# Performance work log

Measured on AMD Instinct MI355X. Metric: run time of the kernel, lower is better.

## Reference

```python
import jax, jax.numpy as jnp
import numpy as np

DIM = 1536
NH = 12
HD = DIM // NH  # 128
F_, H_, W_ = 16, 16, 16
L = F_ * H_ * W_  # 4096


def _precompute_freqs(dim, max_positions, base=10000.0):
    # [max_positions, dim//2] angles
    half = dim // 2
    inv = 1.0 / base ** (np.arange(0, half * 2, 2, dtype=np.float32) / (half * 2))
    pos = np.arange(max_positions, dtype=np.float32)
    return pos[:, None] * inv[None, :]


def _get_3d_freqs(head_dim, F, H, W, base=10000.0):
    half_hd = head_dim // 2
    n_t = max(1, head_dim // 4 // 2)
    n_h = max(1, head_dim * 3 // 8 // 2)
    n_w = half_hd - n_t - n_h
    ft = _precompute_freqs(n_t * 2, F, base)  # [F, n_t]
    fh = _precompute_freqs(n_h * 2, H, base)  # [H, n_h]
    fw = _precompute_freqs(n_w * 2, W, base)  # [W, n_w]
    f_idx = np.broadcast_to(ft[:, None, None, :], (F, H, W, n_t))
    h_idx = np.broadcast_to(fh[None, :, None, :], (F, H, W, n_h))
    w_idx = np.broadcast_to(fw[None, None, :, :], (F, H, W, n_w))
    return np.concatenate([f_idx, h_idx, w_idx], axis=-1).reshape(F * H * W, half_hd)


def setup_inputs() -> dict:
    key = jax.random.key(0)
    ks = jax.random.split(key, 9)
    s = 1.0 / np.sqrt(DIM)
    x = jax.random.normal(ks[0], (1, L, DIM), dtype=jnp.float32)
    freqs = jnp.asarray(_get_3d_freqs(HD, F_, H_, W_), dtype=jnp.float32)
    Wq = jax.random.normal(ks[1], (DIM, DIM), dtype=jnp.float32) * s
    bq = jax.random.normal(ks[2], (DIM,), dtype=jnp.float32) * 0.01
    Wk = jax.random.normal(ks[3], (DIM, DIM), dtype=jnp.float32) * s
    bk = jax.random.normal(ks[4], (DIM,), dtype=jnp.float32) * 0.01
    Wv = jax.random.normal(ks[5], (DIM, DIM), dtype=jnp.float32) * s
    bv = jax.random.normal(ks[6], (DIM,), dtype=jnp.float32) * 0.01
    Wo = jax.random.normal(ks[7], (DIM, DIM), dtype=jnp.float32) * s
    bo = jax.random.normal(ks[8], (DIM,), dtype=jnp.float32) * 0.01
    return {"x": x, "freqs": freqs, "Wq": Wq, "bq": bq, "Wk": Wk, "bk": bk,
            "Wv": Wv, "bv": bv, "Wo": Wo, "bo": bo}


def _apply_rotary(t, cos_v, sin_v):
    # t: [B, Nh, L, Hd]; cos_v/sin_v: [L, Hd//2]
    B, Nh, Lq, Hd = t.shape
    t2 = t.reshape(B, Nh, Lq, Hd // 2, 2)
    x0, x1 = t2[..., 0], t2[..., 1]
    r0 = x0 * cos_v - x1 * sin_v
    r1 = x0 * sin_v + x1 * cos_v
    return jnp.stack([r0, r1], axis=-1).reshape(B, Nh, Lq, Hd)


def reference(x, freqs, Wq, bq, Wk, bk, Wv, bv, Wo, bo):
    B, Lq, D = x.shape
    Nh, Hd = NH, D // NH
    q = (x @ Wq + bq).reshape(B, Lq, Nh, Hd).transpose(0, 2, 1, 3)
    k = (x @ Wk + bk).reshape(B, Lq, Nh, Hd).transpose(0, 2, 1, 3)
    v = (x @ Wv + bv).reshape(B, Lq, Nh, Hd).transpose(0, 2, 1, 3)
    cos_v = jnp.cos(freqs)  # [L, Hd//2]
    sin_v = jnp.sin(freqs)
    q = _apply_rotary(q, cos_v, sin_v)
    k = _apply_rotary(k, cos_v, sin_v)
    scale = 1.0 / jnp.sqrt(jnp.asarray(Hd, dtype=x.dtype))
    scores = jnp.einsum('bhqd,bhkd->bhqk', q, k) * scale
    attn = jax.nn.softmax(scores, axis=-1)
    out = jnp.einsum('bhqk,bhkd->bhqd', attn, v)
    out = out.transpose(0, 2, 1, 3).reshape(B, Lq, D)
    return out @ Wo + bo
```

## Files before the change

### kernel.cpp

```cpp
#include <hip/hip_runtime.h>

#define DIM 1536
#define NH  12
#define HD  128
#define SEQ 4096

typedef unsigned short u16;
typedef unsigned int   u32;
typedef __attribute__((ext_vector_type(8))) short bf16x8;
typedef __attribute__((ext_vector_type(4))) float f32x4;
typedef __attribute__((ext_vector_type(16))) float f32x16;

static __device__ __forceinline__ u16 f2bf(float f) {
    u32 u = __float_as_uint(f);
    u32 r = u + 0x7FFFu + ((u >> 16) & 1u);
    return (u16)(r >> 16);
}
static __device__ __forceinline__ float bf2f(u16 h) {
    return __uint_as_float(((u32)h) << 16);
}
static __device__ __forceinline__ u32 pack2(float a, float b) {
    return (u32)f2bf(a) | ((u32)f2bf(b) << 16);
}

#define GLL(g, s) __builtin_amdgcn_global_load_lds( \
    (const __attribute__((address_space(1))) void*)(g), \
    (__attribute__((address_space(3))) void*)(s), 16, 0, 0)

__global__ __launch_bounds__(256) void k_cvt_x(const float* __restrict__ x, u16* __restrict__ xb) {
    int gid = blockIdx.x * 256 + threadIdx.x;
    const float4* p = (const float4*)x + (size_t)gid * 2;
    float4 a = p[0], b = p[1];
    uint4 o;
    o.x = pack2(a.x, a.y); o.y = pack2(a.z, a.w);
    o.z = pack2(b.x, b.y); o.w = pack2(b.z, b.w);
    *(uint4*)(xb + (size_t)gid * 8) = o;
}

__global__ __launch_bounds__(256) void k_transpose_w(const float* __restrict__ Wq, const float* __restrict__ Wk,
                                                     const float* __restrict__ Wv, const float* __restrict__ Wo,
                                                     u16* __restrict__ wqkv, u16* __restrict__ wot) {
    __shared__ float tile[32][33];
    int z = blockIdx.z;
    const float* W = z == 0 ? Wq : z == 1 ? Wk : z == 2 ? Wv : Wo;
    u16* out = z < 3 ? (wqkv + (size_t)z * DIM * DIM) : wot;
    int tx = threadIdx.x, ty = threadIdx.y;
    int c0 = blockIdx.x * 32, r0 = blockIdx.y * 32;
#pragma unroll
    for (int i = 0; i < 4; i++)
        tile[ty + i * 8][tx] = W[(size_t)(r0 + ty + i * 8) * DIM + c0 + tx];
    __syncthreads();
#pragma unroll
    for (int i = 0; i < 4; i++)
        out[(size_t)(c0 + ty + i * 8) * DIM + r0 + tx] = f2bf(tile[tx][ty + i * 8]);
}

__global__ __launch_bounds__(256) void k_tr_v(const u16* __restrict__ vb, u16* __restrict__ vt) {
    __shared__ u16 tile[32][33];
    int h = blockIdx.z;
    int l0 = blockIdx.x * 32, d0 = blockIdx.y * 32;
    int tx = threadIdx.x, ty = threadIdx.y;
    const u16* src = vb + (size_t)h * SEQ * HD;
    u16* dst = vt + (size_t)h * HD * SEQ;
#pragma unroll
    for (int i = 0; i < 4; i++)
        tile[ty + i * 8][tx] = src[(size_t)(l0 + ty + i * 8) * HD + d0 + tx];
    __syncthreads();
#pragma unroll
    for (int i = 0; i < 4; i++)
        dst[(size_t)(d0 + ty + i * 8) * SEQ + l0 + tx] = tile[tx][ty + i * 8];
}

__global__ __launch_bounds__(256) void k_prep(const float* __restrict__ fr, const float* __restrict__ bq,
                                              const float* __restrict__ bk, const float* __restrict__ bv,
                                              float2* __restrict__ cs, float* __restrict__ bqkv) {
    int gid = blockIdx.x * 256 + threadIdx.x;
    float f = fr[gid];
    cs[gid] = make_float2(cosf(f), sinf(f));
    if (gid < 3 * DIM)
        bqkv[gid] = gid < DIM ? bq[gid] : gid < 2 * DIM ? bk[gid - DIM] : bv[gid - 2 * DIM];
}

__global__ __launch_bounds__(256, 3) void k_gemm(const u16* __restrict__ A, const u16* __restrict__ B,
                                                 const float* __restrict__ bias, int Kdim, int mode,
                                                 u16* __restrict__ qo, u16* __restrict__ ko,
                                                 u16* __restrict__ vo, float* __restrict__ outf) {
    __shared__ u16 As[2][128 * 32];
    __shared__ u16 Bs[2][192 * 32];
    const int tid = threadIdx.x;
    const int w = tid >> 6, l = tid & 63;
    const int wr = w >> 1, wc = w & 1;
    const int lr = l & 15, lg = l >> 4;
    int nwg = gridDim.x * gridDim.y;
    int bid = blockIdx.y * gridDim.x + blockIdx.x;
    int swz = (bid & 7) * (nwg >> 3) + (bid >> 3);
    const int m0 = (swz / gridDim.x) * 128, n0 = (swz % gridDim.x) * 192;
    f32x4 acc[4][6] = {};

    const int srow = l >> 2;
    const int scol = (((l & 3) * 16) ^ (((l >> 2) & 3) << 4)) >> 1;
    const size_t Ab0 = (size_t)(m0 + (w * 2 + 0) * 16 + srow) * Kdim + scol;
    const size_t Ab1 = (size_t)(m0 + (w * 2 + 1) * 16 + srow) * Kdim + scol;
    const size_t Bb0 = (size_t)(n0 + (w * 3 + 0) * 16 + srow) * Kdim + scol;
    const size_t Bb1 = (size_t)(n0 + (w * 3 + 1) * 16 + srow) * Kdim + scol;
    const size_t Bb2 = (size_t)(n0 + (w * 3 + 2) * 16 + srow) * Kdim + scol;
    const int ao0 = (w * 2 + 0) * 512, ao1 = (w * 2 + 1) * 512;
    const int bo0 = (w * 3 + 0) * 512, bo1 = (w * 3 + 1) * 512, bo2 = (w * 3 + 2) * 512;

#define STAGE(buf, kt) do { \
        GLL(A + Ab0 + (kt), As[buf] + ao0); \
        GLL(A + Ab1 + (kt), As[buf] + ao1); \
        GLL(B + Bb0 + (kt), Bs[buf] + bo0); \
        GLL(B + Bb1 + (kt), Bs[buf] + bo1); \
        GLL(B + Bb2 + (kt), Bs[buf] + bo2); \
    } while (0)

    const int nk = Kdim >> 5;
    STAGE(0, 0);
    __syncthreads();

    int cur = 0;
    for (int t = 0; t < nk; ++t) {
        if (t + 1 < nk) STAGE(cur ^ 1, (t + 1) << 5);
        const u16* Ac = As[cur];
        const u16* Bc = Bs[cur];
        const int co = (lg * 8) ^ ((lr & 3) << 3);
        bf16x8 af[4], bg[6];
#pragma unroll
        for (int i = 0; i < 4; i++)
            af[i] = *(const bf16x8*)(Ac + (wr * 64 + i * 16 + lr) * 32 + co);
#pragma unroll
        for (int j = 0; j < 6; j++)
            bg[j] = *(const bf16x8*)(Bc + (wc * 96 + j * 16 + lr) * 32 + co);
#pragma unroll
        for (int i = 0; i < 4; i++)
#pragma unroll
            for (int j = 0; j < 6; j++)
                acc[i][j] = __builtin_amdgcn_mfma_f32_16x16x32_bf16(af[i], bg[j], acc[i][j], 0, 0, 0);
        __syncthreads();
        cur ^= 1;
    }
#undef STAGE

#pragma unroll
    for (int j = 0; j < 6; j++) {
        int gc = n0 + wc * 96 + j * 16 + lr;
        float bb = bias[gc];
#pragma unroll
        for (int i = 0; i < 4; i++) {
            int gr0 = m0 + wr * 64 + i * 16 + lg * 4;
            if (mode == 0) {
                int t = gc / DIM;
                int rr = gc % DIM;
                int hh = rr >> 7, hd = rr & 127;
                u16* dst = t == 0 ? qo : t == 1 ? ko : vo;
                size_t base = (size_t)hh * SEQ * HD + hd;
#pragma unroll
                for (int r = 0; r < 4; r++)
                    dst[base + (size_t)(gr0 + r) * HD] = f2bf(acc[i][j][r] + bb);
            } else {
#pragma unroll
                for (int r = 0; r < 4; r++)
                    outf[(size_t)(gr0 + r) * DIM + gc] = acc[i][j][r] + bb;
            }
        }
    }
}

__global__ __launch_bounds__(256) void k_rope(u16* __restrict__ qb, u16* __restrict__ kb,
                                              const float2* __restrict__ cs) {
    int gid = blockIdx.x * 256 + threadIdx.x;
    const int T = NH * SEQ * 8;
    u16* buf = gid < T ? qb : kb;
    int r = gid < T ? gid : gid - T;
    int hh = r / (SEQ * 8);
    int rr = r % (SEQ * 8);
    int ll = rr >> 3, i0 = (rr & 7) * 8;
    size_t off = ((size_t)hh * SEQ + ll) * HD + 2 * i0;
    uint4 pa = *(const uint4*)(buf + off);
    uint4 pb = *(const uint4*)(buf + off + 8);
    const float4* cp = (const float4*)(cs + (size_t)ll * 64 + i0);
    float4 c0 = cp[0], c1 = cp[1], c2 = cp[2], c3 = cp[3];
    auto rot = [](u32 pk, float cv, float sv) -> u32 {
        float x0 = bf2f((u16)(pk & 0xFFFFu)), x1 = bf2f((u16)(pk >> 16));
        return pack2(x0 * cv - x1 * sv, x0 * sv + x1 * cv);
    };
    uint4 oa, ob;
    oa.x = rot(pa.x, c0.x, c0.y); oa.y = rot(pa.y, c0.z, c0.w);
    oa.z = rot(pa.z, c1.x, c1.y); oa.w = rot(pa.w, c1.z, c1.w);
    ob.x = rot(pb.x, c2.x, c2.y); ob.y = rot(pb.y, c2.z, c2.w);
    ob.z = rot(pb.z, c3.x, c3.y); ob.w = rot(pb.w, c3.z, c3.w);
    *(uint4*)(buf + off) = oa;
    *(uint4*)(buf + off + 8) = ob;
}

__global__ __launch_bounds__(256, 3) void k_attn(const u16* __restrict__ qb, const u16* __restrict__ kbuf,
                                                 const u16* __restrict__ vt, u16* __restrict__ attnb) {
    __shared__ u16 Ks[64 * 128];
    __shared__ u16 Vs[128 * 64];
    __shared__ float MB[128][18];
    const int tid = threadIdx.x;
    const int w = tid >> 6, l = tid & 63;
    const int qh = w & 1, kh = w >> 1;
    const int g = l >> 5, qlane = l & 31;
    const int lr = l & 15, lg = l >> 4;
    int bid = blockIdx.x;
    int gw = (bid & 7) * 96 + (bid >> 3);
    const int h = gw >> 6;
    const int q0 = (gw & 63) << 6;
    const size_t hb = (size_t)h * SEQ * HD;
    constexpr float SCL2 = 0.08838834764831845f * 1.4426950408889634f;
    constexpr float THR = 5.0f;

    const int vrow8 = l >> 3;
    const int vc0 = (((l & 7) * 16) ^ (vrow8 << 4)) >> 1;

    bf16x8 qf[8];
    {
        const u16* qp = qb + hb + (size_t)(q0 + qh * 32 + qlane) * HD + g * 8;
#pragma unroll
        for (int s = 0; s < 8; s++)
            qf[s] = *(const bf16x8*)(qp + s * 16);
    }
    f32x16 O[4] = {};
    float m_run = -1e30f, lsum = 0.f;

    const int krow = kh * 32 + qlane;
    const int ksw = (krow & 7) << 4;
    const int vswl = (qlane & 7) << 4;

    for (int kt = 0; kt < SEQ; kt += 64) {
        __syncthreads();
#pragma unroll
        for (int c = 0; c < 4; c++) {
            int cc = w * 4 + c;
            int key = cc * 4 + lg;
            int kd0 = ((lr * 16) ^ ((key & 7) << 4)) >> 1;
            GLL(kbuf + hb + (size_t)(kt + key) * HD + kd0, Ks + cc * 512);
            int dd = cc * 8 + vrow8;
            GLL(vt + hb + (size_t)dd * SEQ + kt + vc0, Vs + cc * 512);
        }
        __syncthreads();

        f32x16 ST = {};
        const u16* Kp = Ks + krow * 128;
#pragma unroll
        for (int s = 0; s < 8; s++) {
            bf16x8 kf = *(const bf16x8*)(Kp + (((s * 32 + g * 16) ^ ksw) >> 1));
            ST = __builtin_amdgcn_mfma_f32_32x32x16_bf16(kf, qf[s], ST, 0, 0, 0);
        }

        float mx = ST[0];
#pragma unroll
        for (int r = 1; r < 16; r++) mx = fmaxf(mx, ST[r]);
        mx = fmaxf(mx, __shfl_xor(mx, 32));
        float mt = mx * SCL2;
        bool grow = mt > m_run + THR;
        float m_new = grow ? mt : m_run;
        if (__any(grow)) {
            float alpha = grow ? __builtin_amdgcn_exp2f(m_run - m_new) : 1.0f;
            lsum *= alpha;
            m_run = m_new;
#pragma unroll
            for (int db = 0; db < 4; db++)
#pragma unroll
                for (int r = 0; r < 16; r++) O[db][r] *= alpha;
        }
        float ps = 0.f;
#pragma unroll
        for (int r = 0; r < 16; r++) {
            float p = __builtin_amdgcn_exp2f(fmaf(ST[r], SCL2, -m_new));
            ST[r] = p; ps += p;
        }
        lsum += ps;

        u32 pw[2][4];
#pragma unroll
        for (int s2 = 0; s2 < 2; s2++) {
            int rb = s2 * 8;
            u32 a, b2, c2, d2;
            asm("v_cvt_pk_bf16_f32 %0, %1, %2" : "=v"(a)  : "v"(ST[rb + 0]), "v"(ST[rb + 1]));
            asm("v_cvt_pk_bf16_f32 %0, %1, %2" : "=v"(b2) : "v"(ST[rb + 2]), "v"(ST[rb + 3]));
            asm("v_cvt_pk_bf16_f32 %0, %1, %2" : "=v"(c2) : "v"(ST[rb + 4]), "v"(ST[rb + 5]));
            asm("v_cvt_pk_bf16_f32 %0, %1, %2" : "=v"(d2) : "v"(ST[rb + 6]), "v"(ST[rb + 7]));
            asm("v_permlane32_swap_b32 %0, %1" : "+v"(a), "+v"(c2));
            asm("v_permlane32_swap_b32 %0, %1" : "+v"(b2), "+v"(d2));
            pw[s2][0] = a; pw[s2][1] = b2; pw[s2][2] = c2; pw[s2][3] = d2;
        }

#pragma unroll
        for (int s2 = 0; s2 < 2; s2++) {
            union { u32 u[4]; bf16x8 v; } pf;
            pf.u[0] = pw[s2][0]; pf.u[1] = pw[s2][1]; pf.u[2] = pw[s2][2]; pf.u[3] = pw[s2][3];
            int kb2 = kh * 64 + s2 * 32 + g * 16;
#pragma unroll
            for (int db = 0; db < 4; db++) {
                int d = db * 32 + qlane;
                bf16x8 vf = *(const bf16x8*)(Vs + d * 64 + ((kb2 ^ vswl) >> 1));
                O[db] = __builtin_amdgcn_mfma_f32_32x32x16_bf16(vf, pf.v, O[db], 0, 0, 0);
            }
        }
    }

    lsum += __shfl_xor(lsum, 32);

    const int row = qh * 64 + l;
    u16* op = attnb + (size_t)(q0 + qh * 32 + qlane) * DIM + h * HD;
    __syncthreads();
    if (kh == 1) { MB[row][16] = m_run; MB[row][17] = lsum; }
    __syncthreads();
    float a0 = 0.f, a1 = 0.f;
    if (kh == 0) {
        float m1 = MB[row][16], l1 = MB[row][17];
        float mM = fmaxf(m_run, m1);
        a0 = __builtin_amdgcn_exp2f(m_run - mM);
        a1 = __builtin_amdgcn_exp2f(m1 - mM);
        float linv = 1.0f / (lsum * a0 + l1 * a1);
        a0 *= linv; a1 *= linv;
    }
#pragma unroll
    for (int db = 0; db < 4; db++) {
        __syncthreads();
        if (kh == 1) {
#pragma unroll
            for (int r = 0; r < 16; r++) MB[row][r] = O[db][r];
        }
        __syncthreads();
        if (kh == 0) {
#pragma unroll
            for (int r = 0; r < 16; r++) {
                int d = db * 32 + (r & 3) + 8 * (r >> 2) + 4 * g;
                op[d] = f2bf(O[db][r] * a0 + MB[row][r] * a1);
            }
        }
    }
}

extern "C" void kernel_launch(void* const* d_in, const int* in_sizes, int n_in,
                              void* d_out, int out_size, void* d_ws, size_t ws_size,
                              hipStream_t stream) {
    (void)in_sizes; (void)n_in; (void)out_size; (void)ws_size;
    const float* x  = (const float*)d_in[0];
    const float* fr = (const float*)d_in[1];
    const float* Wq = (const float*)d_in[2];
    const float* bq = (const float*)d_in[3];
    const float* Wk = (const float*)d_in[4];
    const float* bk = (const float*)d_in[5];
    const float* Wv = (const float*)d_in[6];
    const float* bv = (const float*)d_in[7];
    const float* Wo = (const float*)d_in[8];
    const float* bo = (const float*)d_in[9];
    float* out = (float*)d_out;

    char* ws = (char*)d_ws;
    size_t off = 0;
    auto alloc = [&](size_t b) { char* p = ws + off; off = (off + b + 255) & ~(size_t)255; return p; };
    u16*   xb    = (u16*)alloc((size_t)SEQ * DIM * 2);
    u16*   wqkv  = (u16*)alloc((size_t)3 * DIM * DIM * 2);
    u16*   wot   = (u16*)alloc((size_t)DIM * DIM * 2);
    float* bqkv  = (float*)alloc((size_t)3 * DIM * 4);
    u16*   qb    = (u16*)alloc((size_t)SEQ * DIM * 2);
    u16*   kb    = (u16*)alloc((size_t)SEQ * DIM * 2);
    u16*   vb    = (u16*)alloc((size_t)SEQ * DIM * 2);
    u16*   vtb   = (u16*)alloc((size_t)SEQ * DIM * 2);
    u16*   attnb = (u16*)alloc((size_t)SEQ * DIM * 2);
    float2* cs   = (float2*)alloc((size_t)SEQ * 64 * 8);

    k_cvt_x<<<3072, 256, 0, stream>>>(x, xb);
    k_transpose_w<<<dim3(48, 48, 4), dim3(32, 8), 0, stream>>>(Wq, Wk, Wv, Wo, wqkv, wot);
    k_prep<<<1024, 256, 0, stream>>>(fr, bq, bk, bv, cs, bqkv);
    k_gemm<<<dim3(24, 32), 256, 0, stream>>>(xb, wqkv, bqkv, DIM, 0, qb, kb, vb, nullptr);
    k_rope<<<3072, 256, 0, stream>>>(qb, kb, cs);
    k_tr_v<<<dim3(128, 4, 12), dim3(32, 8), 0, stream>>>(vb, vtb);
    k_attn<<<768, 256, 0, stream>>>(qb, kb, vtb, attnb);
    k_gemm<<<dim3(8, 32), 256, 0, stream>>>(attnb, wot, bo, DIM, 1, nullptr, nullptr, nullptr, out);
}
```

Baseline: 271.1 us.

## Fuse RoPE, softmax scale, and V transpose into QKV GEMM epilogue

```diff
diff --git a/kernel.cpp b/kernel.cpp
--- a/kernel.cpp
+++ b/kernel.cpp
@@ -16,9 +16,6 @@
     u32 r = u + 0x7FFFu + ((u >> 16) & 1u);
     return (u16)(r >> 16);
 }
-static __device__ __forceinline__ float bf2f(u16 h) {
-    return __uint_as_float(((u32)h) << 16);
-}
 static __device__ __forceinline__ u32 pack2(float a, float b) {
     return (u32)f2bf(a) | ((u32)f2bf(b) << 16);
 }
@@ -26,6 +23,8 @@
 #define GLL(g, s) __builtin_amdgcn_global_load_lds( \
     (const __attribute__((address_space(1))) void*)(g), \
     (__attribute__((address_space(3))) void*)(s), 16, 0, 0)
+
+#define SCLQ 0.127532f
 
 __global__ __launch_bounds__(256) void k_cvt_x(const float* __restrict__ x, u16* __restrict__ xb) {
     int gid = blockIdx.x * 256 + threadIdx.x;
@@ -55,22 +54,6 @@
         out[(size_t)(c0 + ty + i * 8) * DIM + r0 + tx] = f2bf(tile[tx][ty + i * 8]);
 }
 
-__global__ __launch_bounds__(256) void k_tr_v(const u16* __restrict__ vb, u16* __restrict__ vt) {
-    __shared__ u16 tile[32][33];
-    int h = blockIdx.z;
-    int l0 = blockIdx.x * 32, d0 = blockIdx.y * 32;
-    int tx = threadIdx.x, ty = threadIdx.y;
-    const u16* src = vb + (size_t)h * SEQ * HD;
-    u16* dst = vt + (size_t)h * HD * SEQ;
-#pragma unroll
-    for (int i = 0; i < 4; i++)
-        tile[ty + i * 8][tx] = src[(size_t)(l0 + ty + i * 8) * HD + d0 + tx];
-    __syncthreads();
-#pragma unroll
-    for (int i = 0; i < 4; i++)
-        dst[(size_t)(d0 + ty + i * 8) * SEQ + l0 + tx] = tile[tx][ty + i * 8];
-}
-
 __global__ __launch_bounds__(256) void k_prep(const float* __restrict__ fr, const float* __restrict__ bq,
                                               const float* __restrict__ bk, const float* __restrict__ bv,
                                               float2* __restrict__ cs, float* __restrict__ bqkv) {
@@ -83,8 +66,9 @@
 
 __global__ __launch_bounds__(256, 3) void k_gemm(const u16* __restrict__ A, const u16* __restrict__ B,
                                                  const float* __restrict__ bias, int Kdim, int mode,
+                                                 const float2* __restrict__ cs2,
                                                  u16* __restrict__ qo, u16* __restrict__ ko,
-                                                 u16* __restrict__ vo, float* __restrict__ outf) {
+                                                 u16* __restrict__ vto, float* __restrict__ outf) {
     __shared__ u16 As[2][128 * 32];
     __shared__ u16 Bs[2][192 * 32];
     const int tid = threadIdx.x;
@@ -153,11 +137,29 @@
                 int t = gc / DIM;
                 int rr = gc % DIM;
                 int hh = rr >> 7, hd = rr & 127;
-                u16* dst = t == 0 ? qo : t == 1 ? ko : vo;
-                size_t base = (size_t)hh * SEQ * HD + hd;
-#pragma unroll
-                for (int r = 0; r < 4; r++)
-                    dst[base + (size_t)(gr0 + r) * HD] = f2bf(acc[i][j][r] + bb);
+                if (t == 2) {
+                    u16* dst = vto + ((size_t)hh * HD + hd) * SEQ + gr0;
+                    ushort4 pk;
+                    pk.x = f2bf(acc[i][j][0] + bb);
+                    pk.y = f2bf(acc[i][j][1] + bb);
+                    pk.z = f2bf(acc[i][j][2] + bb);
+                    pk.w = f2bf(acc[i][j][3] + bb);
+                    *(ushort4*)dst = pk;
+                } else {
+                    bool odd = gc & 1;
+                    u16* dst = (t == 0 ? qo : ko) + (size_t)hh * SEQ * HD + hd;
+                    const float2* cp = cs2 + (hd >> 1);
+#pragma unroll
+                    for (int r = 0; r < 4; r++) {
+                        float v = acc[i][j][r] + bb;
+                        float vp = __shfl_xor(v, 1);
+                        float2 c = cp[(size_t)(gr0 + r) * 64];
+                        float o = odd ? fmaf(vp, c.y, v * c.x)
+                                      : fmaf(v, c.x, -vp * c.y);
+                        if (t == 0) o *= SCLQ;
+                        dst[(size_t)(gr0 + r) * HD] = f2bf(o);
+                    }
+                }
             } else {
 #pragma unroll
                 for (int r = 0; r < 4; r++)
@@ -165,33 +167,6 @@
             }
         }
     }
-}
-
-__global__ __launch_bounds__(256) void k_rope(u16* __restrict__ qb, u16* __restrict__ kb,
-                                              const float2* __restrict__ cs) {
-    int gid = blockIdx.x * 256 + threadIdx.x;
-    const int T = NH * SEQ * 8;
-    u16* buf = gid < T ? qb : kb;
-    int r = gid < T ? gid : gid - T;
-    int hh = r / (SEQ * 8);
-    int rr = r % (SEQ * 8);
-    int ll = rr >> 3, i0 = (rr & 7) * 8;
-    size_t off = ((size_t)hh * SEQ + ll) * HD + 2 * i0;
-    uint4 pa = *(const uint4*)(buf + off);
-    uint4 pb = *(const uint4*)(buf + off + 8);
-    const float4* cp = (const float4*)(cs + (size_t)ll * 64 + i0);
-    float4 c0 = cp[0], c1 = cp[1], c2 = cp[2], c3 = cp[3];
-    auto rot = [](u32 pk, float cv, float sv) -> u32 {
-        float x0 = bf2f((u16)(pk & 0xFFFFu)), x1 = bf2f((u16)(pk >> 16));
-        return pack2(x0 * cv - x1 * sv, x0 * sv + x1 * cv);
-    };
-    uint4 oa, ob;
-    oa.x = rot(pa.x, c0.x, c0.y); oa.y = rot(pa.y, c0.z, c0.w);
-    oa.z = rot(pa.z, c1.x, c1.y); oa.w = rot(pa.w, c1.z, c1.w);
-    ob.x = rot(pb.x, c2.x, c2.y); ob.y = rot(pb.y, c2.z, c2.w);
-    ob.z = rot(pb.z, c3.x, c3.y); ob.w = rot(pb.w, c3.z, c3.w);
-    *(uint4*)(buf + off) = oa;
-    *(uint4*)(buf + off + 8) = ob;
 }
 
 __global__ __launch_bounds__(256, 3) void k_attn(const u16* __restrict__ qb, const u16* __restrict__ kbuf,
@@ -209,7 +184,6 @@
     const int h = gw >> 6;
     const int q0 = (gw & 63) << 6;
     const size_t hb = (size_t)h * SEQ * HD;
-    constexpr float SCL2 = 0.08838834764831845f * 1.4426950408889634f;
     constexpr float THR = 5.0f;
 
     const int vrow8 = l >> 3;
@@ -254,9 +228,8 @@
 #pragma unroll
         for (int r = 1; r < 16; r++) mx = fmaxf(mx, ST[r]);
         mx = fmaxf(mx, __shfl_xor(mx, 32));
-        float mt = mx * SCL2;
-        bool grow = mt > m_run + THR;
-        float m_new = grow ? mt : m_run;
+        bool grow = mx > m_run + THR;
+        float m_new = grow ? mx : m_run;
         if (__any(grow)) {
             float alpha = grow ? __builtin_amdgcn_exp2f(m_run - m_new) : 1.0f;
             lsum *= alpha;
@@ -269,7 +242,7 @@
         float ps = 0.f;
 #pragma unroll
         for (int r = 0; r < 16; r++) {
-            float p = __builtin_amdgcn_exp2f(fmaf(ST[r], SCL2, -m_new));
+            float p = __builtin_amdgcn_exp2f(ST[r] - m_new);
             ST[r] = p; ps += p;
         }
         lsum += ps;
@@ -361,7 +334,6 @@
     float* bqkv  = (float*)alloc((size_t)3 * DIM * 4);
     u16*   qb    = (u16*)alloc((size_t)SEQ * DIM * 2);
     u16*   kb    = (u16*)alloc((size_t)SEQ * DIM * 2);
-    u16*   vb    = (u16*)alloc((size_t)SEQ * DIM * 2);
     u16*   vtb   = (u16*)alloc((size_t)SEQ * DIM * 2);
     u16*   attnb = (u16*)alloc((size_t)SEQ * DIM * 2);
     float2* cs   = (float2*)alloc((size_t)SEQ * 64 * 8);
@@ -369,9 +341,7 @@
     k_cvt_x<<<3072, 256, 0, stream>>>(x, xb);
     k_transpose_w<<<dim3(48, 48, 4), dim3(32, 8), 0, stream>>>(Wq, Wk, Wv, Wo, wqkv, wot);
     k_prep<<<1024, 256, 0, stream>>>(fr, bq, bk, bv, cs, bqkv);
-    k_gemm<<<dim3(24, 32), 256, 0, stream>>>(xb, wqkv, bqkv, DIM, 0, qb, kb, vb, nullptr);
-    k_rope<<<3072, 256, 0, stream>>>(qb, kb, cs);
-    k_tr_v<<<dim3(128, 4, 12), dim3(32, 8), 0, stream>>>(vb, vtb);
+    k_gemm<<<dim3(24, 32), 256, 0, stream>>>(xb, wqkv, bqkv, DIM, 0, cs, qb, kb, vtb, nullptr);
     k_attn<<<768, 256, 0, stream>>>(qb, kb, vtb, attnb);
-    k_gemm<<<dim3(8, 32), 256, 0, stream>>>(attnb, wot, bo, DIM, 1, nullptr, nullptr, nullptr, out);
-}
+    k_gemm<<<dim3(8, 32), 256, 0, stream>>>(attnb, wot, bo, DIM, 1, nullptr, nullptr, nullptr, nullptr, out);
+}
```

New measurement: 259.4 us. 1.04x faster.
